# Performance work log

Measured on AMD Instinct MI355X. Metric: run time of the kernel, lower is better.

Reference implementation:

```python
import jax, jax.numpy as jnp
import numpy as np
import math

B, S, D, H = 4, 4096, 1024, 128

def setup_inputs() -> dict:
    key = jax.random.key(0)
    ks = jax.random.split(key, 4)
    scale = 1.0 / math.sqrt(D)
    return {
        "inputs": jax.random.normal(ks[0], (B, S, D), dtype=jnp.float32),
        "Wk": jax.random.normal(ks[1], (H, D), dtype=jnp.float32) * scale,
        "bk": jnp.zeros((H,), dtype=jnp.float32),
        "Wq": jax.random.normal(ks[2], (H, D), dtype=jnp.float32) * scale,
        "bq": jnp.zeros((H,), dtype=jnp.float32),
        "Wv": jax.random.normal(ks[3], (H, D), dtype=jnp.float32) * scale,
        "bv": jnp.zeros((H,), dtype=jnp.float32),
        "padding_mask": jnp.ones((B, S), dtype=jnp.int32),
    }

def reference(inputs, Wk, bk, Wq, bq, Wv, bv, padding_mask):
    # Linear projections: [B,S,D] x [H,D]^T -> [B,S,H]
    k = jnp.einsum('bsd,hd->bsh', inputs, Wk) + bk
    q = jnp.einsum('bsd,hd->bsh', inputs, Wq) + bq
    v = jnp.einsum('bsd,hd->bsh', inputs, Wv) + bv
    # Scaled dot-product scores: [B,S,S]
    scores = jnp.einsum('bqh,bkh->bqk', q, k) / jnp.sqrt(jnp.float32(k.shape[-1]))
    # Mask out padded key positions (mask==0 -> -1e9), broadcast over query dim
    scores = jnp.where(padding_mask[:, None, :] == 0, jnp.float32(-1e9), scores)
    weights = jax.nn.softmax(scores, axis=-1)
    # Dropout is identity in eval mode (reference runs inference / training=False)
    out = jnp.einsum('bqk,bkh->bqh', weights, v)
    return out
```

## Files before the change

kernel.cpp:

```cpp
#include <hip/hip_runtime.h>
#include <cmath>

#define B_ 4
#define S_ 4096
#define D_ 1024
#define H_ 128
#define M_ (B_*S_)
#define NQT 32

typedef _Float16 half8 __attribute__((ext_vector_type(8)));
typedef _Float16 half4 __attribute__((ext_vector_type(4)));
typedef float f32x4 __attribute__((ext_vector_type(4)));
typedef float f32x16 __attribute__((ext_vector_type(16)));
typedef int i32x4 __attribute__((ext_vector_type(4)));

#define LOG2E 1.44269504088896340f

__device__ __forceinline__ void gload16(const void* g, void* l) {
    __builtin_amdgcn_global_load_lds(
        (const __attribute__((address_space(1))) unsigned int*)g,
        (__attribute__((address_space(3))) unsigned int*)l,
        16, 0, 0);
}

__global__ __launch_bounds__(256) void conv_w(
    const float* __restrict__ Wq, const float* __restrict__ Wk,
    const float* __restrict__ Wv, _Float16* __restrict__ wh)
{
    const int idx  = blockIdx.x * 256 + threadIdx.x;
    const int base = idx * 8;
    const int m    = base >> 17;
    const int off  = base & ((H_ * D_) - 1);
    const float* src = (m == 0 ? Wq : m == 1 ? Wk : Wv) + off;
    const float4 a = ((const float4*)src)[0];
    const float4 c = ((const float4*)src)[1];
    half8 h = { (_Float16)a.x, (_Float16)a.y, (_Float16)a.z, (_Float16)a.w,
                (_Float16)c.x, (_Float16)c.y, (_Float16)c.z, (_Float16)c.w };
    *(half8*)(wh + base) = h;
}

__global__ __launch_bounds__(256, 3) void proj_kernel(
    const float* __restrict__ x, const _Float16* __restrict__ wh,
    const float* __restrict__ bq, const float* __restrict__ bk,
    const float* __restrict__ bv,
    _Float16* __restrict__ qh, _Float16* __restrict__ kh,
    _Float16* __restrict__ vt)
{
    __shared__ _Float16 Xs[2][64][72];
    __shared__ _Float16 Ws2[2][128][64];

    const int t = threadIdx.x;
    const int yb = blockIdx.y;
    const float* __restrict__ bias = (yb == 0) ? bq : (yb == 1) ? bk : bv;
    const int m0 = blockIdx.x * 64;
    const int w = t >> 6, lane = t & 63;
    const int lg = lane >> 4, lr = lane & 15;

    f32x4 acc[8];
    #pragma unroll
    for (int i = 0; i < 8; ++i) acc[i] = f32x4{0.f, 0.f, 0.f, 0.f};

    const int xrow = t >> 2, xc = (t & 3) * 16;
    const float* xbase = x + (size_t)(m0 + xrow) * D_ + xc;

    int wbyte[4];
    #pragma unroll
    for (int i = 0; i < 4; ++i) {
        const int wrow = 32 * w + 8 * i + (lane >> 3);
        const int wblk = (lane & 7) ^ (lane >> 3);
        wbyte[i] = (wrow * D_ + wblk * 8) * 2;
    }
    const char* whb = (const char*)(wh + (size_t)yb * H_ * D_);

    float4 xfA[4], xfB[4];

#define WISSUE(KT, BUF)                                                       \
    {                                                                         \
        const char* wsrc = whb + (KT) * (64 * 2);                             \
        _Pragma("unroll")                                                     \
        for (int i = 0; i < 4; ++i)                                           \
            gload16(wsrc + wbyte[i], &Ws2[BUF][32 * w + 8 * i][0]);           \
    }
#define XISSUE(KT, XS)                                                        \
    {                                                                         \
        const float4* xs_ = (const float4*)(xbase + (KT) * 64);               \
        _Pragma("unroll") for (int i = 0; i < 4; ++i) XS[i] = xs_[i];         \
    }
#define XWRITE(XS, BUF)                                                       \
    {                                                                         \
        _Pragma("unroll") for (int i = 0; i < 4; ++i) {                       \
            half4 h = { (_Float16)XS[i].x, (_Float16)XS[i].y,                 \
                        (_Float16)XS[i].z, (_Float16)XS[i].w };               \
            *(half4*)&Xs[BUF][xrow][xc + 4 * i] = h;                          \
        }                                                                     \
    }
#define PMFMA(BUF)                                                            \
    {                                                                         \
        _Pragma("unroll") for (int kk = 0; kk < 2; ++kk) {                    \
            half8 a = *(const half8*)&Xs[BUF][w * 16 + lr][kk * 32 + 8 * lg]; \
            _Pragma("unroll") for (int ni = 0; ni < 8; ++ni) {                \
                half8 bfr = *(const half8*)&Ws2[BUF][ni * 16 + lr]            \
                                [((4 * kk + lg) ^ (lr & 7)) * 8];             \
                acc[ni] = __builtin_amdgcn_mfma_f32_16x16x32_f16(a, bfr, acc[ni], 0, 0, 0); \
            }                                                                 \
        }                                                                     \
    }

    WISSUE(0, 0)
    XISSUE(0, xfA)
    XISSUE(1, xfB)
    XWRITE(xfA, 0)
    __syncthreads();

    for (int kt = 0; kt < 16; kt += 2) {
        WISSUE(kt + 1, 1)
        if (kt + 2 < 16) XISSUE(kt + 2, xfA)
        PMFMA(0)
        XWRITE(xfB, 1)
        __syncthreads();
        if (kt + 2 < 16) WISSUE(kt + 2, 0)
        if (kt + 3 < 16) XISSUE(kt + 3, xfB)
        PMFMA(1)
        if (kt + 2 < 16) XWRITE(xfA, 0)
        __syncthreads();
    }
#undef WISSUE
#undef XISSUE
#undef XWRITE
#undef PMFMA

    const float qscale = 0.08838834764831845f * LOG2E;
    const int rowb = m0 + w * 16 + lg * 4;
    #pragma unroll
    for (int ni = 0; ni < 8; ++ni) {
        const int col = ni * 16 + lr;
        const float bval = bias[col];
        if (yb == 0) {
            #pragma unroll
            for (int r = 0; r < 4; ++r)
                qh[(size_t)(rowb + r) * H_ + col] = (_Float16)((acc[ni][r] + bval) * qscale);
        } else if (yb == 1) {
            #pragma unroll
            for (int r = 0; r < 4; ++r)
                kh[(size_t)(rowb + r) * H_ + col] = (_Float16)(acc[ni][r] + bval);
        } else {
            const int bb = rowb >> 12, s0 = rowb & (S_ - 1);
            half4 h;
            #pragma unroll
            for (int r = 0; r < 4; ++r) h[r] = (_Float16)(acc[ni][r] + bval);
            *(half4*)&vt[(size_t)bb * H_ * S_ + (size_t)col * S_ + s0] = h;
        }
    }
}

__device__ __forceinline__ void attn_tile32(
    const _Float16 (&Kb)[64][128], const _Float16 (&Vb)[128][64],
    const half8 (&qf)[8], f32x16 (&acc2)[4], float& m_, float& l_,
    int muse, int lane)
{
    const unsigned long long bz = __ballot(muse == 0);
    const int l31 = lane & 31, l7 = lane & 7, hi = lane >> 5;

    f32x16 sf[2];
    #pragma unroll
    for (int nb = 0; nb < 2; ++nb)
        #pragma unroll
        for (int r = 0; r < 16; ++r) sf[nb][r] = 0.f;
    #pragma unroll
    for (int kt = 0; kt < 8; ++kt) {
        #pragma unroll
        for (int nb = 0; nb < 2; ++nb) {
            half8 kb = *(const half8*)&Kb[nb * 32 + l31][((2 * kt + hi) ^ l7) * 8];
            sf[nb] = __builtin_amdgcn_mfma_f32_32x32x16_f16(kb, qf[kt], sf[nb], 0, 0, 0);
        }
    }
    if (bz) {
        #pragma unroll
        for (int nb = 0; nb < 2; ++nb)
            #pragma unroll
            for (int r = 0; r < 16; ++r) {
                const int kv = nb * 32 + (r & 3) + 8 * (r >> 2) + 4 * hi;
                if ((bz >> kv) & 1ull) sf[nb][r] = -3e9f;
            }
    }
    float tmax = sf[0][0];
    #pragma unroll
    for (int nb = 0; nb < 2; ++nb)
        #pragma unroll
        for (int r = 0; r < 16; ++r) tmax = fmaxf(tmax, sf[nb][r]);
    tmax = fmaxf(tmax, __shfl_xor(tmax, 32));
    if (!__all(tmax <= m_ + 8.f)) {
        const float mn  = fmaxf(m_, tmax);
        const float scl = exp2f(m_ - mn);
        m_ = mn; l_ *= scl;
        #pragma unroll
        for (int hb = 0; hb < 4; ++hb) acc2[hb] *= scl;
    }
    float rsum = 0.f;
    #pragma unroll
    for (int nb = 0; nb < 2; ++nb)
        #pragma unroll
        for (int r = 0; r < 16; ++r) {
            const float p = exp2f(sf[nb][r] - m_);
            sf[nb][r] = p;
            rsum += p;
        }
    rsum += __shfl_xor(rsum, 32);
    l_ += rsum;

    int pkw[2][8];
    #pragma unroll
    for (int nb = 0; nb < 2; ++nb)
        #pragma unroll
        for (int i = 0; i < 8; ++i) {
            auto h2 = __builtin_amdgcn_cvt_pkrtz(sf[nb][2 * i], sf[nb][2 * i + 1]);
            pkw[nb][i] = __builtin_bit_cast(int, h2);
        }
    #pragma unroll
    for (int nb = 0; nb < 2; ++nb)
        #pragma unroll
        for (int hf = 0; hf < 2; ++hf) {
            const int i0 = hf * 4;
            const int sA = hi ? pkw[nb][i0 + 0] : pkw[nb][i0 + 2];
            const int sB = hi ? pkw[nb][i0 + 1] : pkw[nb][i0 + 3];
            const int rA = __shfl_xor(sA, 32);
            const int rB = __shfl_xor(sB, 32);
            const int n0 = hi ? rA : pkw[nb][i0 + 0];
            const int n1 = hi ? rB : pkw[nb][i0 + 1];
            const int n2 = hi ? pkw[nb][i0 + 2] : rA;
            const int n3 = hi ? pkw[nb][i0 + 3] : rB;
            pkw[nb][i0 + 0] = n0; pkw[nb][i0 + 1] = n1;
            pkw[nb][i0 + 2] = n2; pkw[nb][i0 + 3] = n3;
        }
    #pragma unroll
    for (int s = 0; s < 4; ++s) {
        const int nb = s >> 1, hf = s & 1;
        const half8 pb = __builtin_bit_cast(half8,
            i32x4{ pkw[nb][hf * 4 + 0], pkw[nb][hf * 4 + 1],
                   pkw[nb][hf * 4 + 2], pkw[nb][hf * 4 + 3] });
        #pragma unroll
        for (int hb = 0; hb < 4; ++hb) {
            half8 vb = *(const half8*)&Vb[hb * 32 + l31][((2 * s + hi) ^ l7) * 8];
            acc2[hb] = __builtin_amdgcn_mfma_f32_32x32x16_f16(vb, pb, acc2[hb], 0, 0, 0);
        }
    }
}

__global__ __launch_bounds__(256, 2) void attn_kernel(
    const _Float16* __restrict__ qh, const _Float16* __restrict__ kh,
    const _Float16* __restrict__ vt, const int* __restrict__ mask,
    float* __restrict__ pout, float* __restrict__ pm, float* __restrict__ pl,
    const int nsplit)
{
    __shared__ _Float16 Ks[2][64][128];
    __shared__ _Float16 Vs[2][128][64];

    const int t = threadIdx.x;
    const int id = blockIdx.x;
    int qt, sp, b;
    const int ncombo = B_ * nsplit;
    if ((ncombo & 7) == 0) {
        const int per_xcd = ncombo >> 3;
        const int j = id >> 3;
        qt = j & (NQT - 1);
        const int combo = (id & 7) * per_xcd + (j >> 5);
        sp = combo % nsplit; b = combo / nsplit;
    } else {
        qt = id & (NQT - 1);
        const int rest = id >> 5;
        sp = rest % nsplit; b = rest / nsplit;
    }
    const int q0 = qt * 128;
    const int w = t >> 6, lane = t & 63;
    const int l31 = lane & 31, hi = lane >> 5;
    const int kvlen  = S_ / nsplit;
    const int iters  = kvlen >> 6;
    const int kvbase = sp * kvlen;

    int kbyte[4], vbyte[4];
    #pragma unroll
    for (int i = 0; i < 4; ++i) {
        const int krow = 16 * w + 4 * i + (lane >> 4);
        const int kblk = (lane & 15) ^ (krow & 7);
        kbyte[i] = (krow * H_ + kblk * 8) * 2;
        const int vrow = 32 * w + 8 * i + (lane >> 3);
        const int vblk = (lane & 7) ^ (lane >> 3);
        vbyte[i] = (vrow * S_ + vblk * 8) * 2;
    }
    const char* kbase_b = (const char*)(kh + (size_t)(b * S_ + kvbase) * H_);
    const char* vbase_b = (const char*)(vt + (size_t)b * H_ * S_ + kvbase);
    const char* mbase_b = (const char*)(mask + b * S_ + kvbase + lane);

#define ISSUE_TILE(IT, NB)                                                    \
    {                                                                         \
        const char* kb_t = kbase_b + (size_t)(IT) * (64 * H_ * 2);            \
        const char* vb_t = vbase_b + (size_t)(IT) * (64 * 2);                 \
        _Pragma("unroll")                                                     \
        for (int i = 0; i < 4; ++i)                                           \
            gload16(kb_t + kbyte[i], &Ks[NB][16 * w + 4 * i][0]);             \
        _Pragma("unroll")                                                     \
        for (int i = 0; i < 4; ++i)                                           \
            gload16(vb_t + vbyte[i], &Vs[NB][32 * w + 8 * i][0]);             \
    }

    half8 qf[8];
    {
        const _Float16* qp = qh + (size_t)(b * S_ + q0 + 32 * w + l31) * H_ + 8 * hi;
        #pragma unroll
        for (int kt = 0; kt < 8; ++kt) qf[kt] = *(const half8*)(qp + 16 * kt);
    }

    float m_ = -1e30f, l_ = 0.f;
    f32x16 acc2[4];
    #pragma unroll
    for (int hb = 0; hb < 4; ++hb)
        #pragma unroll
        for (int r = 0; r < 16; ++r) acc2[hb][r] = 0.f;

    ISSUE_TILE(0, 0)
    int mA = *(const int*)mbase_b;
    int mB = 0;
    __syncthreads();

    for (int it = 0; it < iters; it += 2) {
        if (it + 1 < iters) {
            ISSUE_TILE(it + 1, 1)
            mB = *(const int*)(mbase_b + (size_t)(it + 1) * 256);
        }
        attn_tile32(Ks[0], Vs[0], qf, acc2, m_, l_, mA, lane);
        __syncthreads();
        if (it + 2 < iters) {
            ISSUE_TILE(it + 2, 0)
            mA = *(const int*)(mbase_b + (size_t)(it + 2) * 256);
        }
        if (it + 1 < iters)
            attn_tile32(Ks[1], Vs[1], qf, acc2, m_, l_, mB, lane);
        __syncthreads();
    }
#undef ISSUE_TILE

    const int qrow = b * S_ + q0 + 32 * w + l31;
    float* op = pout + (size_t)(sp * M_ + qrow) * H_;
    #pragma unroll
    for (int hb = 0; hb < 4; ++hb)
        #pragma unroll
        for (int i = 0; i < 8; ++i) {
            const int h = hb * 32 + 2 * (i & 1) + 8 * (i >> 1) + 4 * hi;
            float2 v2 = make_float2(acc2[hb][2 * i], acc2[hb][2 * i + 1]);
            *(float2*)(op + h) = v2;
        }
    if (hi == 0) {
        pm[sp * M_ + qrow] = m_;
        pl[sp * M_ + qrow] = l_;
    }
}

__global__ __launch_bounds__(256) void combine_kernel(
    const float* __restrict__ pout, const float* __restrict__ pm,
    const float* __restrict__ pl, float* __restrict__ out, const int nsplit)
{
    const int idx = blockIdx.x * 256 + threadIdx.x;
    const int row = idx >> 7;
    const int h   = idx & (H_ - 1);
    float M = -1e30f;
    for (int sp = 0; sp < nsplit; ++sp) M = fmaxf(M, pm[sp * M_ + row]);
    float Z = 0.f, o = 0.f;
    for (int sp = 0; sp < nsplit; ++sp) {
        const float wgt = exp2f(pm[sp * M_ + row] - M);
        Z += wgt * pl[sp * M_ + row];
        o += wgt * pout[(size_t)(sp * M_ + row) * H_ + h];
    }
    out[idx] = o / Z;
}

extern "C" void kernel_launch(void* const* d_in, const int* in_sizes, int n_in,
                              void* d_out, int out_size, void* d_ws, size_t ws_size,
                              hipStream_t stream)
{
    (void)in_sizes; (void)n_in; (void)out_size;
    const float* x  = (const float*)d_in[0];
    const float* Wk = (const float*)d_in[1];
    const float* bk = (const float*)d_in[2];
    const float* Wq = (const float*)d_in[3];
    const float* bq = (const float*)d_in[4];
    const float* Wv = (const float*)d_in[5];
    const float* bv = (const float*)d_in[6];
    const int* mask = (const int*)d_in[7];

    char* ws = (char*)d_ws;
    const size_t qkvBytes = (size_t)M_ * H_ * sizeof(_Float16);
    _Float16* qh = (_Float16*)ws;
    _Float16* kh = (_Float16*)(ws + qkvBytes);
    _Float16* vt = (_Float16*)(ws + 2 * qkvBytes);
    _Float16* wh = (_Float16*)(ws + 3 * qkvBytes);
    const size_t whBytes = (size_t)3 * H_ * D_ * sizeof(_Float16);
    char* rest = ws + 3 * qkvBytes + whBytes;

    int nsplit = 4;
    const size_t perSplit = (size_t)M_ * H_ * 4 + 2 * (size_t)M_ * 4;
    while (nsplit > 1 &&
           3 * qkvBytes + whBytes + (size_t)nsplit * perSplit > ws_size) nsplit >>= 1;

    float* pout = (float*)rest;
    float* pm   = (float*)(rest + (size_t)nsplit * M_ * H_ * 4);
    float* pl   = pm + (size_t)nsplit * M_;

    conv_w<<<dim3(3 * H_ * D_ / (256 * 8)), 256, 0, stream>>>(Wq, Wk, Wv, wh);
    proj_kernel<<<dim3(M_ / 64, 3), 256, 0, stream>>>(x, wh, bq, bk, bv, qh, kh, vt);
    attn_kernel<<<dim3(NQT * B_ * nsplit), 256, 0, stream>>>(qh, kh, vt, mask, pout, pm, pl, nsplit);
    combine_kernel<<<dim3(M_ * H_ / 256), 256, 0, stream>>>(pout, pm, pl, (float*)d_out, nsplit);
}
```

Before: 109.9 us.

## Single-buffer attention K/V tiles, raise occupancy to 3 blocks, and double KV splits

```diff
diff --git a/kernel.cpp b/kernel.cpp
--- a/kernel.cpp
+++ b/kernel.cpp
@@ -246,14 +246,14 @@
     }
 }
 
-__global__ __launch_bounds__(256, 2) void attn_kernel(
+__global__ __launch_bounds__(256, 3) void attn_kernel(
     const _Float16* __restrict__ qh, const _Float16* __restrict__ kh,
     const _Float16* __restrict__ vt, const int* __restrict__ mask,
     float* __restrict__ pout, float* __restrict__ pm, float* __restrict__ pl,
     const int nsplit)
 {
-    __shared__ _Float16 Ks[2][64][128];
-    __shared__ _Float16 Vs[2][128][64];
+    __shared__ _Float16 Ks[64][128];
+    __shared__ _Float16 Vs[128][64];
 
     const int t = threadIdx.x;
     const int id = blockIdx.x;
@@ -291,16 +291,16 @@
     const char* vbase_b = (const char*)(vt + (size_t)b * H_ * S_ + kvbase);
     const char* mbase_b = (const char*)(mask + b * S_ + kvbase + lane);
 
-#define ISSUE_TILE(IT, NB)                                                    \
+#define ISSUE_TILE(IT)                                                        \
     {                                                                         \
         const char* kb_t = kbase_b + (size_t)(IT) * (64 * H_ * 2);            \
         const char* vb_t = vbase_b + (size_t)(IT) * (64 * 2);                 \
         _Pragma("unroll")                                                     \
         for (int i = 0; i < 4; ++i)                                           \
-            gload16(kb_t + kbyte[i], &Ks[NB][16 * w + 4 * i][0]);             \
+            gload16(kb_t + kbyte[i], &Ks[16 * w + 4 * i][0]);                 \
         _Pragma("unroll")                                                     \
         for (int i = 0; i < 4; ++i)                                           \
-            gload16(vb_t + vbyte[i], &Vs[NB][32 * w + 8 * i][0]);             \
+            gload16(vb_t + vbyte[i], &Vs[32 * w + 8 * i][0]);                 \
     }
 
     half8 qf[8];
@@ -317,25 +317,12 @@
         #pragma unroll
         for (int r = 0; r < 16; ++r) acc2[hb][r] = 0.f;
 
-    ISSUE_TILE(0, 0)
-    int mA = *(const int*)mbase_b;
-    int mB = 0;
-    __syncthreads();
-
-    for (int it = 0; it < iters; it += 2) {
-        if (it + 1 < iters) {
-            ISSUE_TILE(it + 1, 1)
-            mB = *(const int*)(mbase_b + (size_t)(it + 1) * 256);
-        }
-        attn_tile32(Ks[0], Vs[0], qf, acc2, m_, l_, mA, lane);
+    for (int it = 0; it < iters; ++it) {
+        if (it) __syncthreads();
+        ISSUE_TILE(it)
+        const int mreg = *(const int*)(mbase_b + (size_t)it * 256);
         __syncthreads();
-        if (it + 2 < iters) {
-            ISSUE_TILE(it + 2, 0)
-            mA = *(const int*)(mbase_b + (size_t)(it + 2) * 256);
-        }
-        if (it + 1 < iters)
-            attn_tile32(Ks[1], Vs[1], qf, acc2, m_, l_, mB, lane);
-        __syncthreads();
+        attn_tile32(Ks, Vs, qf, acc2, m_, l_, mreg, lane);
     }
 #undef ISSUE_TILE
 
@@ -396,7 +383,7 @@
     const size_t whBytes = (size_t)3 * H_ * D_ * sizeof(_Float16);
     char* rest = ws + 3 * qkvBytes + whBytes;
 
-    int nsplit = 4;
+    int nsplit = 8;
     const size_t perSplit = (size_t)M_ * H_ * 4 + 2 * (size_t)M_ * 4;
     while (nsplit > 1 &&
            3 * qkvBytes + whBytes + (size_t)nsplit * perSplit > ws_size) nsplit >>= 1;
```

After: 135.9 us. 1.24x slower.

## Deepen K/V prefetch with explicit vmcnt waits and raise MFMA priority

Applied to the files above, without the earlier changes.

```diff
diff --git a/kernel.cpp b/kernel.cpp
--- a/kernel.cpp
+++ b/kernel.cpp
@@ -166,6 +166,7 @@
     for (int nb = 0; nb < 2; ++nb)
         #pragma unroll
         for (int r = 0; r < 16; ++r) sf[nb][r] = 0.f;
+    __builtin_amdgcn_s_setprio(1);
     #pragma unroll
     for (int kt = 0; kt < 8; ++kt) {
         #pragma unroll
@@ -174,6 +175,7 @@
             sf[nb] = __builtin_amdgcn_mfma_f32_32x32x16_f16(kb, qf[kt], sf[nb], 0, 0, 0);
         }
     }
+    __builtin_amdgcn_s_setprio(0);
     if (bz) {
         #pragma unroll
         for (int nb = 0; nb < 2; ++nb)
@@ -183,12 +185,14 @@
                 if ((bz >> kv) & 1ull) sf[nb][r] = -3e9f;
             }
     }
-    float tmax = sf[0][0];
-    #pragma unroll
-    for (int nb = 0; nb < 2; ++nb)
-        #pragma unroll
-        for (int r = 0; r < 16; ++r) tmax = fmaxf(tmax, sf[nb][r]);
-    tmax = fmaxf(tmax, __shfl_xor(tmax, 32));
+    float tv[16];
+    #pragma unroll
+    for (int r = 0; r < 16; ++r) tv[r] = fmaxf(sf[0][r], sf[1][r]);
+    #pragma unroll
+    for (int off = 8; off > 0; off >>= 1)
+        #pragma unroll
+        for (int r = 0; r < off; ++r) tv[r] = fmaxf(tv[r], tv[r + off]);
+    float tmax = fmaxf(tv[0], __shfl_xor(tv[0], 32));
     if (!__all(tmax <= m_ + 8.f)) {
         const float mn  = fmaxf(m_, tmax);
         const float scl = exp2f(m_ - mn);
@@ -196,17 +200,18 @@
         #pragma unroll
         for (int hb = 0; hb < 4; ++hb) acc2[hb] *= scl;
     }
-    float rsum = 0.f;
     #pragma unroll
     for (int nb = 0; nb < 2; ++nb)
         #pragma unroll
-        for (int r = 0; r < 16; ++r) {
-            const float p = exp2f(sf[nb][r] - m_);
-            sf[nb][r] = p;
-            rsum += p;
-        }
-    rsum += __shfl_xor(rsum, 32);
-    l_ += rsum;
+        for (int r = 0; r < 16; ++r) sf[nb][r] = exp2f(sf[nb][r] - m_);
+    float sv[16];
+    #pragma unroll
+    for (int r = 0; r < 16; ++r) sv[r] = sf[0][r] + sf[1][r];
+    #pragma unroll
+    for (int off = 8; off > 0; off >>= 1)
+        #pragma unroll
+        for (int r = 0; r < off; ++r) sv[r] += sv[r + off];
+    l_ += sv[0] + __shfl_xor(sv[0], 32);
 
     int pkw[2][8];
     #pragma unroll
@@ -232,6 +237,7 @@
             pkw[nb][i0 + 0] = n0; pkw[nb][i0 + 1] = n1;
             pkw[nb][i0 + 2] = n2; pkw[nb][i0 + 3] = n3;
         }
+    __builtin_amdgcn_s_setprio(1);
     #pragma unroll
     for (int s = 0; s < 4; ++s) {
         const int nb = s >> 1, hf = s & 1;
@@ -244,6 +250,7 @@
             acc2[hb] = __builtin_amdgcn_mfma_f32_32x32x16_f16(vb, pb, acc2[hb], 0, 0, 0);
         }
     }
+    __builtin_amdgcn_s_setprio(0);
 }
 
 __global__ __launch_bounds__(256, 2) void attn_kernel(
@@ -291,7 +298,7 @@
     const char* vbase_b = (const char*)(vt + (size_t)b * H_ * S_ + kvbase);
     const char* mbase_b = (const char*)(mask + b * S_ + kvbase + lane);
 
-#define ISSUE_TILE(IT, NB)                                                    \
+#define ISSUE_TILE(IT, NB, MRECV)                                             \
     {                                                                         \
         const char* kb_t = kbase_b + (size_t)(IT) * (64 * H_ * 2);            \
         const char* vb_t = vbase_b + (size_t)(IT) * (64 * 2);                 \
@@ -301,7 +308,11 @@
         _Pragma("unroll")                                                     \
         for (int i = 0; i < 4; ++i)                                           \
             gload16(vb_t + vbyte[i], &Vs[NB][32 * w + 8 * i][0]);             \
-    }
+        MRECV = *(const int*)(mbase_b + (size_t)(IT) * 256);                  \
+    }
+#define WAIT9  asm volatile("s_waitcnt vmcnt(9)" ::: "memory")
+#define WAIT0  asm volatile("s_waitcnt vmcnt(0)" ::: "memory")
+#define BAR    asm volatile("s_barrier" ::: "memory")
 
     half8 qf[8];
     {
@@ -317,27 +328,28 @@
         #pragma unroll
         for (int r = 0; r < 16; ++r) acc2[hb][r] = 0.f;
 
-    ISSUE_TILE(0, 0)
-    int mA = *(const int*)mbase_b;
-    int mB = 0;
-    __syncthreads();
+    int mA, mB;
+    ISSUE_TILE(0, 0, mA)
+    ISSUE_TILE(1, 1, mB)
+    WAIT9;
+    BAR;
 
     for (int it = 0; it < iters; it += 2) {
-        if (it + 1 < iters) {
-            ISSUE_TILE(it + 1, 1)
-            mB = *(const int*)(mbase_b + (size_t)(it + 1) * 256);
-        }
         attn_tile32(Ks[0], Vs[0], qf, acc2, m_, l_, mA, lane);
-        __syncthreads();
-        if (it + 2 < iters) {
-            ISSUE_TILE(it + 2, 0)
-            mA = *(const int*)(mbase_b + (size_t)(it + 2) * 256);
-        }
-        if (it + 1 < iters)
-            attn_tile32(Ks[1], Vs[1], qf, acc2, m_, l_, mB, lane);
-        __syncthreads();
+        BAR;
+        if (it + 2 < iters) { ISSUE_TILE(it + 2, 0, mA) WAIT9; }
+        else                { WAIT0; }
+        BAR;
+        attn_tile32(Ks[1], Vs[1], qf, acc2, m_, l_, mB, lane);
+        BAR;
+        if (it + 3 < iters) { ISSUE_TILE(it + 3, 1, mB) WAIT9; }
+        else                { WAIT0; }
+        BAR;
     }
 #undef ISSUE_TILE
+#undef WAIT9
+#undef WAIT0
+#undef BAR
 
     const int qrow = b * S_ + q0 + 32 * w + l31;
     float* op = pout + (size_t)(sp * M_ + qrow) * H_;
```

Result: slower. 113.2 us (+3.0%).
